# Performance work log

Hardware: AMD Instinct MI355X
Metric: run time of the kernel (lower is better)

The kernel has to match this reference:

```python
import jax, jax.numpy as jnp
import numpy as np

B, S, D, H = 8, 1024, 768, 16
PD = D // H  # projection dims per head


def setup_inputs() -> dict:
    key = jax.random.key(0)
    ks = jax.random.split(key, 9)
    s = 1.0 / np.sqrt(D)
    return {
        "inputs": jax.random.normal(ks[0], (B, S, D), dtype=jnp.float32),
        "Wq": jax.random.normal(ks[1], (D, D), dtype=jnp.float32) * s,
        "bq": jnp.zeros((D,), dtype=jnp.float32),
        "Wk": jax.random.normal(ks[2], (D, D), dtype=jnp.float32) * s,
        "bk": jnp.zeros((D,), dtype=jnp.float32),
        "Wv": jax.random.normal(ks[3], (D, D), dtype=jnp.float32) * s,
        "bv": jnp.zeros((D,), dtype=jnp.float32),
        "Wo": jax.random.normal(ks[4], (D, D), dtype=jnp.float32) * s,
        "bo": jnp.zeros((D,), dtype=jnp.float32),
    }


def _split_heads(x):
    # [B,S,D] -> [B,H,S,PD]
    return x.reshape(B, S, H, PD).transpose(0, 2, 1, 3)


def reference(inputs, Wq, bq, Wk, bk, Wv, bv, Wo, bo):
    q = _split_heads(inputs @ Wq + bq)
    k = _split_heads(inputs @ Wk + bk)
    v = _split_heads(inputs @ Wv + bv)
    scale = 1.0 / jnp.sqrt(jnp.asarray(PD, dtype=q.dtype))
    scores = jnp.einsum("bhqd,bhkd->bhqk", q, k) * scale
    weights = jax.nn.softmax(scores, axis=-1)
    attn = jnp.einsum("bhqk,bhkd->bhqd", weights, v)
    concat = attn.transpose(0, 2, 1, 3).reshape(B, S, D)
    return concat @ Wo + bo
```

## Files before the change

kernel.cpp:

```cpp
#include <hip/hip_runtime.h>
#include <hip/hip_bf16.h>

#define B_   8
#define S_   1024
#define D_   768
#define H_   16
#define PD_  48
#define PDP  64
#define M_   8192
#define BH_  128

#define QSCALE 0.20823031f

typedef __attribute__((ext_vector_type(8))) short short8;
typedef __attribute__((ext_vector_type(4))) float floatx4;

__device__ __forceinline__ unsigned short f2bf(float f) {
    return (unsigned short)((__float_as_uint(f) + 0x8000u) >> 16);
}
__device__ __forceinline__ unsigned int pack_bf2(float lo, float hi) {
    unsigned a = __float_as_uint(hi) + 0x8000u;
    unsigned b = __float_as_uint(lo) + 0x8000u;
    return __builtin_amdgcn_perm(a, b, 0x07060302u);
}

__device__ __forceinline__ void async_copy16(const unsigned short* gptr, unsigned short* lptr) {
    __builtin_amdgcn_global_load_lds(
        (const __attribute__((address_space(1))) unsigned int*)gptr,
        (__attribute__((address_space(3))) unsigned int*)lptr, 16, 0, 0);
}

__global__ __launch_bounds__(256) void prep_kernel(
    const float* __restrict__ X, unsigned short* __restrict__ Xb,
    const float* __restrict__ w0, const float* __restrict__ w1,
    const float* __restrict__ w2, const float* __restrict__ w3,
    unsigned short* __restrict__ Wtall) {
    __shared__ float tile[32][33];
    const int tid = threadIdx.x;
    const int bx = blockIdx.x;
    if (bx < 6144) {
        long i = ((long)bx * 256 + tid) * 4;
        float4 v = *(const float4*)(X + i);
        uint2 o;
        o.x = pack_bf2(v.x, v.y);
        o.y = pack_bf2(v.z, v.w);
        *(uint2*)(Xb + i) = o;
        return;
    }
    const int t = bx - 6144;
    const int z = t / 576, r = t % 576;
    const int nt = (r % 24) * 32, kt = (r / 24) * 32;
    const int tx = tid & 31, ty = tid >> 5;
    const float* W = (z == 0) ? w0 : (z == 1) ? w1 : (z == 2) ? w2 : w3;
    unsigned short* Wt = Wtall + (long)z * D_ * D_;
#pragma unroll
    for (int i = 0; i < 4; i++)
        tile[ty + i * 8][tx] = W[(long)(kt + ty + i * 8) * D_ + nt + tx];
    __syncthreads();
#pragma unroll
    for (int i = 0; i < 4; i++)
        Wt[(long)(nt + ty + i * 8) * D_ + kt + tx] = f2bf(tile[tx][ty + i * 8]);
}

__device__ __forceinline__ void gemm_core(
    const unsigned short* __restrict__ Ag,
    const unsigned short* __restrict__ Btg,
    unsigned short* Asm, unsigned short* Bsm, floatx4 acc[4][4]) {
    const int tid = threadIdx.x;
    const int lane = tid & 63, w = tid >> 6;
    const int wr = (w >> 1) * 64, wc = (w & 1) * 64;
    const int l15 = lane & 15, l4 = lane >> 4;
    const floatx4 zero = {0.f, 0.f, 0.f, 0.f};
#pragma unroll
    for (int mt = 0; mt < 4; mt++)
#pragma unroll
        for (int nt = 0; nt < 4; nt++) acc[mt][nt] = zero;

    for (int kb = 0; kb < D_; kb += 64) {
#pragma unroll
        for (int i = 0; i < 4; i++) {
            int c = tid + i * 256;
            int row = c >> 3, seg = (c & 7) ^ (row & 7);
            long goff = (long)row * D_ + kb + seg * 8;
            async_copy16(&Ag[goff], &Asm[c * 8]);
            async_copy16(&Btg[goff], &Bsm[c * 8]);
        }
        __syncthreads();
#pragma unroll
        for (int kk = 0; kk < 2; kk++) {
            short8 af[4], bf[4];
#pragma unroll
            for (int mt = 0; mt < 4; mt++) {
                int r = wr + mt * 16 + l15;
                af[mt] = *(const short8*)&Asm[r * 64 + (((kk * 4 + l4) ^ (r & 7)) * 8)];
            }
#pragma unroll
            for (int nt = 0; nt < 4; nt++) {
                int c = wc + nt * 16 + l15;
                bf[nt] = *(const short8*)&Bsm[c * 64 + (((kk * 4 + l4) ^ (c & 7)) * 8)];
            }
#pragma unroll
            for (int mt = 0; mt < 4; mt++)
#pragma unroll
                for (int nt = 0; nt < 4; nt++)
                    acc[mt][nt] = __builtin_amdgcn_mfma_f32_16x16x32_bf16(
                        af[mt], bf[nt], acc[mt][nt], 0, 0, 0);
        }
        __syncthreads();
    }
}

__global__ __launch_bounds__(256) void gemm_qkv_kernel(
    const unsigned short* __restrict__ Xb, const unsigned short* __restrict__ Wtall,
    const float* __restrict__ bq, const float* __restrict__ bk,
    const float* __restrict__ bv, unsigned short* __restrict__ QKV) {
    __shared__ __align__(16) unsigned short Asm[128 * 64];
    __shared__ __align__(16) unsigned short Bsm[128 * 64];
    const int z = blockIdx.z;
    const int m0 = blockIdx.x * 128, n0 = blockIdx.y * 128;
    const float* bias = (z == 0) ? bq : (z == 1) ? bk : bv;
    const float vscale = (z == 0) ? QSCALE : 1.0f;
    floatx4 acc[4][4];
    gemm_core(Xb + (long)m0 * D_, Wtall + (long)z * D_ * D_ + (long)n0 * D_, Asm, Bsm, acc);

    unsigned short* out = QKV + (long)z * BH_ * S_ * PDP;
    const int tid = threadIdx.x, lane = tid & 63, w = tid >> 6;
    const int wr = (w >> 1) * 64, wc = (w & 1) * 64;
    const int l15 = lane & 15, l4 = lane >> 4;
    const int b = m0 >> 10, sbase = m0 & 1023;
#pragma unroll
    for (int nt = 0; nt < 4; nt++) {
        int n = n0 + wc + nt * 16 + l15;
        int h = n / PD_, pd = n % PD_;
        float bb = bias[n];
#pragma unroll
        for (int mt = 0; mt < 4; mt++) {
#pragma unroll
            for (int r = 0; r < 4; r++) {
                int s = sbase + wr + mt * 16 + l4 * 4 + r;
                out[((long)(b * H_ + h) * S_ + s) * PDP + pd] = f2bf((acc[mt][nt][r] + bb) * vscale);
            }
        }
    }
}

__global__ __launch_bounds__(256) void transpose_v_kernel(
    const unsigned short* __restrict__ V, unsigned short* __restrict__ Vt) {
    __shared__ __align__(16) unsigned short T[64 * 64];
    const int tid = threadIdx.x;
    const int st = blockIdx.x * 64, bh = blockIdx.y;
    const unsigned short* src = V + (long)bh * S_ * PDP;
    unsigned short* dst = Vt + (long)bh * PDP * S_;
#pragma unroll
    for (int i = 0; i < 2; i++) {
        int c = tid + i * 256;
        int row = c >> 3, seg = (c & 7) ^ (row & 7);
        async_copy16(&src[(long)(st + row) * PDP + seg * 8], &T[c * 8]);
    }
    __syncthreads();
    const int d = tid >> 2;
    unsigned short tmp[16];
#pragma unroll
    for (int j = 0; j < 16; j++) {
        int sl = (tid & 3) * 16 + j;
        unsigned short v = T[sl * 64 + ((d >> 3) ^ (sl & 7)) * 8 + (d & 7)];
        tmp[j] = (d < PD_) ? v : ((d == PD_) ? (unsigned short)0x3F80 : (unsigned short)0);
    }
    *(uint4*)&dst[(long)d * S_ + st + (tid & 3) * 16] = *(uint4*)&tmp[0];
    *(uint4*)&dst[(long)d * S_ + st + (tid & 3) * 16 + 8] = *(uint4*)&tmp[8];
}

__global__ __launch_bounds__(256) void gemm_out_kernel(
    const unsigned short* __restrict__ Ctx, const unsigned short* __restrict__ Wot,
    const float* __restrict__ bo, float* __restrict__ Out) {
    __shared__ __align__(16) unsigned short Asm[128 * 64];
    __shared__ __align__(16) unsigned short Bsm[128 * 64];
    const int m0 = blockIdx.x * 128, n0 = blockIdx.y * 128;
    floatx4 acc[4][4];
    gemm_core(Ctx + (long)m0 * D_, Wot + (long)n0 * D_, Asm, Bsm, acc);

    const int tid = threadIdx.x, lane = tid & 63, w = tid >> 6;
    const int wr = (w >> 1) * 64, wc = (w & 1) * 64;
    const int l15 = lane & 15, l4 = lane >> 4;
#pragma unroll
    for (int nt = 0; nt < 4; nt++) {
        int n = n0 + wc + nt * 16 + l15;
        float bb = bo[n];
#pragma unroll
        for (int mt = 0; mt < 4; mt++) {
#pragma unroll
            for (int r = 0; r < 4; r++) {
                int m = m0 + wr + mt * 16 + l4 * 4 + r;
                Out[(long)m * D_ + n] = acc[mt][nt][r] + bb;
            }
        }
    }
}

__global__ __launch_bounds__(256) void attn_kernel(
    const unsigned short* __restrict__ Qg, const unsigned short* __restrict__ Kg,
    const unsigned short* __restrict__ Vtg, unsigned short* __restrict__ Ctx) {
    __shared__ __align__(16) unsigned short Ps[4][64 * 64];
    const int tid = threadIdx.x, lane = tid & 63, w = tid >> 6;
    const int l15 = lane & 15, l4 = lane >> 4;
    const int bh = blockIdx.x, qt = blockIdx.y;
    const long qkbase = (long)bh * S_ * PDP;
    const long vbase  = (long)bh * PDP * S_;

    short8 bq[4][2];
#pragma unroll
    for (int g = 0; g < 4; g++) {
        int qrow = qt * 256 + w * 64 + g * 16 + l15;
        bq[g][0] = *(const short8*)&Qg[qkbase + (long)qrow * PDP + l4 * 8];
        bq[g][1] = *(const short8*)&Qg[qkbase + (long)qrow * PDP + 32 + l4 * 8];
    }
    if (l4 >= 2) {
        const short8 z8 = {0, 0, 0, 0, 0, 0, 0, 0};
#pragma unroll
        for (int g = 0; g < 4; g++) bq[g][1] = z8;
    }

    const floatx4 zero = {0.f, 0.f, 0.f, 0.f};
    floatx4 accO[4][4];
#pragma unroll
    for (int g = 0; g < 4; g++)
#pragma unroll
        for (int nt = 0; nt < 4; nt++) accO[g][nt] = zero;

    unsigned short* Pw = &Ps[w][0];

    for (int kt = 0; kt < 16; kt++) {
        short8 ak[4][2];
#pragma unroll
        for (int ks = 0; ks < 4; ks++) {
            const unsigned short* kr = &Kg[qkbase + (long)(kt * 64 + ks * 16 + l15) * PDP];
            ak[ks][0] = *(const short8*)&kr[l4 * 8];
            ak[ks][1] = *(const short8*)&kr[32 + l4 * 8];
        }

#pragma unroll
        for (int g = 0; g < 4; g++) {
            floatx4 sc[4];
#pragma unroll
            for (int ks = 0; ks < 4; ks++) {
                floatx4 a = zero;
                a = __builtin_amdgcn_mfma_f32_16x16x32_bf16(ak[ks][0], bq[g][0], a, 0, 0, 0);
                a = __builtin_amdgcn_mfma_f32_16x16x32_bf16(ak[ks][1], bq[g][1], a, 0, 0, 0);
                sc[ks] = a;
            }
            int prow = g * 16 + l15;
#pragma unroll
            for (int ks = 0; ks < 4; ks++) {
                uint2 pp;
                pp.x = pack_bf2(__builtin_amdgcn_exp2f(sc[ks][0]),
                                __builtin_amdgcn_exp2f(sc[ks][1]));
                pp.y = pack_bf2(__builtin_amdgcn_exp2f(sc[ks][2]),
                                __builtin_amdgcn_exp2f(sc[ks][3]));
                int addr = prow * 64 + (((ks * 2 + (l4 >> 1)) ^ (prow & 7)) * 8) + (l4 & 1) * 4;
                *(uint2*)&Pw[addr] = pp;
            }
        }

#pragma unroll
        for (int kk = 0; kk < 2; kk++) {
            short8 bv[4];
#pragma unroll
            for (int nt = 0; nt < 4; nt++) {
                int d = nt * 16 + l15;
                bv[nt] = *(const short8*)&Vtg[vbase + (long)d * S_ + kt * 64 + kk * 32 + l4 * 8];
            }
#pragma unroll
            for (int g = 0; g < 4; g++) {
                int prow = g * 16 + l15;
                short8 ap = *(const short8*)&Pw[prow * 64 + (((kk * 4 + l4) ^ (prow & 7)) * 8)];
#pragma unroll
                for (int nt = 0; nt < 4; nt++)
                    accO[g][nt] = __builtin_amdgcn_mfma_f32_16x16x32_bf16(ap, bv[nt], accO[g][nt], 0, 0, 0);
            }
        }
    }

    const int b = bh >> 4, h = bh & 15;
#pragma unroll
    for (int g = 0; g < 4; g++) {
#pragma unroll
        for (int r = 0; r < 4; r++) {
            float lsum = __shfl(accO[g][3][r], lane & 48);
            float inv = 1.0f / lsum;
            int q = qt * 256 + w * 64 + g * 16 + l4 * 4 + r;
            long rowoff = (long)(b * S_ + q) * D_ + h * PD_;
#pragma unroll
            for (int nt = 0; nt < 3; nt++)
                Ctx[rowoff + nt * 16 + l15] = f2bf(accO[g][nt][r] * inv);
        }
    }
}

extern "C" void kernel_launch(void* const* d_in, const int* in_sizes, int n_in,
                              void* d_out, int out_size, void* d_ws, size_t ws_size,
                              hipStream_t stream) {
    const float* X  = (const float*)d_in[0];
    const float* Wq = (const float*)d_in[1];
    const float* bq = (const float*)d_in[2];
    const float* Wk = (const float*)d_in[3];
    const float* bk = (const float*)d_in[4];
    const float* Wv = (const float*)d_in[5];
    const float* bv = (const float*)d_in[6];
    const float* Wo = (const float*)d_in[7];
    const float* bo = (const float*)d_in[8];

    unsigned char* ws = (unsigned char*)d_ws;
    const long XB_BYTES  = (long)M_ * D_ * 2;
    const long WT_BYTES  = (long)D_ * D_ * 2;
    const long QKV_BYTES = (long)BH_ * S_ * PDP * 2;

    unsigned short* Xbf   = (unsigned short*)(ws);
    unsigned short* Wtall = (unsigned short*)(ws + XB_BYTES);
    unsigned short* Qws   = (unsigned short*)(ws + XB_BYTES + 4 * WT_BYTES);
    unsigned short* Kws   = Qws + QKV_BYTES / 2;
    unsigned short* Vws   = Kws + QKV_BYTES / 2;
    unsigned short* Vtws  = Vws + QKV_BYTES / 2;
    unsigned short* Ctx   = Vws;

    prep_kernel<<<8448, 256, 0, stream>>>(X, Xbf, Wq, Wk, Wv, Wo, Wtall);
    gemm_qkv_kernel<<<dim3(64, 6, 3), 256, 0, stream>>>(Xbf, Wtall, bq, bk, bv, Qws);
    transpose_v_kernel<<<dim3(16, 128), 256, 0, stream>>>(Vws, Vtws);
    attn_kernel<<<dim3(128, 4), 256, 0, stream>>>(Qws, Kws, Vtws, Ctx);
    gemm_out_kernel<<<dim3(64, 6), 256, 0, stream>>>(
        Ctx, Wtall + 3 * (WT_BYTES / 2), bo, (float*)d_out);
}
```

Before: 223.4 us.

## Stage K/V tiles in LDS with double buffering and vectorize epilogue stores

The attention kernel now loads K and V^T tiles cooperatively into double-buffered, XOR-swizzled shared memory using async copies, prefetching the next tile while the current one is computed. Previously each wave read K and V^T directly from global memory. MFMA operands are swapped in the GEMMs and in the PV product so each lane holds four consecutive columns of a row, which lets the QKV, output and context epilogues use vectorized 8- or 16-byte stores instead of scalar ones. This adds 32KB of LDS and a barrier per iteration, and sets launch_bounds to 2 blocks per CU, which may limit occupancy.

```diff
diff --git a/kernel.cpp b/kernel.cpp
--- a/kernel.cpp
+++ b/kernel.cpp
@@ -104,7 +104,7 @@
 #pragma unroll
                 for (int nt = 0; nt < 4; nt++)
                     acc[mt][nt] = __builtin_amdgcn_mfma_f32_16x16x32_bf16(
-                        af[mt], bf[nt], acc[mt][nt], 0, 0, 0);
+                        bf[nt], af[mt], acc[mt][nt], 0, 0, 0);
         }
         __syncthreads();
     }
@@ -130,16 +130,17 @@
     const int b = m0 >> 10, sbase = m0 & 1023;
 #pragma unroll
     for (int nt = 0; nt < 4; nt++) {
-        int n = n0 + wc + nt * 16 + l15;
-        int h = n / PD_, pd = n % PD_;
-        float bb = bias[n];
+        int nq = n0 + wc + nt * 16 + l4 * 4;
+        int h = nq / PD_, pd0 = nq % PD_;
+        float4 bb = *(const float4*)&bias[nq];
+        long hbase = (long)(b * H_ + h) * S_;
 #pragma unroll
         for (int mt = 0; mt < 4; mt++) {
-#pragma unroll
-            for (int r = 0; r < 4; r++) {
-                int s = sbase + wr + mt * 16 + l4 * 4 + r;
-                out[((long)(b * H_ + h) * S_ + s) * PDP + pd] = f2bf((acc[mt][nt][r] + bb) * vscale);
-            }
+            int s = sbase + wr + mt * 16 + l15;
+            uint2 pp;
+            pp.x = pack_bf2((acc[mt][nt][0] + bb.x) * vscale, (acc[mt][nt][1] + bb.y) * vscale);
+            pp.y = pack_bf2((acc[mt][nt][2] + bb.z) * vscale, (acc[mt][nt][3] + bb.w) * vscale);
+            *(uint2*)&out[(hbase + s) * PDP + pd0] = pp;
         }
     }
 }
@@ -184,22 +185,24 @@
     const int l15 = lane & 15, l4 = lane >> 4;
 #pragma unroll
     for (int nt = 0; nt < 4; nt++) {
-        int n = n0 + wc + nt * 16 + l15;
-        float bb = bo[n];
+        int nq = n0 + wc + nt * 16 + l4 * 4;
+        float4 bb = *(const float4*)&bo[nq];
 #pragma unroll
         for (int mt = 0; mt < 4; mt++) {
-#pragma unroll
-            for (int r = 0; r < 4; r++) {
-                int m = m0 + wr + mt * 16 + l4 * 4 + r;
-                Out[(long)m * D_ + n] = acc[mt][nt][r] + bb;
-            }
-        }
-    }
-}
-
-__global__ __launch_bounds__(256) void attn_kernel(
+            int m = m0 + wr + mt * 16 + l15;
+            float4 o;
+            o.x = acc[mt][nt][0] + bb.x; o.y = acc[mt][nt][1] + bb.y;
+            o.z = acc[mt][nt][2] + bb.z; o.w = acc[mt][nt][3] + bb.w;
+            *(float4*)&Out[(long)m * D_ + nq] = o;
+        }
+    }
+}
+
+__global__ __launch_bounds__(256, 2) void attn_kernel(
     const unsigned short* __restrict__ Qg, const unsigned short* __restrict__ Kg,
     const unsigned short* __restrict__ Vtg, unsigned short* __restrict__ Ctx) {
+    __shared__ __align__(16) unsigned short Ks[2][64 * 64];
+    __shared__ __align__(16) unsigned short Vs[2][64 * 64];
     __shared__ __align__(16) unsigned short Ps[4][64 * 64];
     const int tid = threadIdx.x, lane = tid & 63, w = tid >> 6;
     const int l15 = lane & 15, l4 = lane >> 4;
@@ -207,6 +210,15 @@
     const long qkbase = (long)bh * S_ * PDP;
     const long vbase  = (long)bh * PDP * S_;
 
+    const int c0 = tid, c1 = tid + 256;
+    const int row0 = c0 >> 3, seg0 = (c0 & 7) ^ (row0 & 7);
+    const int row1 = c1 >> 3, seg1 = (c1 & 7) ^ (row1 & 7);
+
+    async_copy16(&Kg[qkbase + (long)row0 * PDP + seg0 * 8], &Ks[0][c0 * 8]);
+    async_copy16(&Kg[qkbase + (long)row1 * PDP + seg1 * 8], &Ks[0][c1 * 8]);
+    async_copy16(&Vtg[vbase + (long)row0 * S_ + seg0 * 8], &Vs[0][c0 * 8]);
+    async_copy16(&Vtg[vbase + (long)row1 * S_ + seg1 * 8], &Vs[0][c1 * 8]);
+
     short8 bq[4][2];
 #pragma unroll
     for (int g = 0; g < 4; g++) {
@@ -230,12 +242,24 @@
     unsigned short* Pw = &Ps[w][0];
 
     for (int kt = 0; kt < 16; kt++) {
+        const int cur = kt & 1;
+        __syncthreads();
+        if (kt < 15) {
+            const int nb = cur ^ 1;
+            const long krow = qkbase + (long)(kt + 1) * 64 * PDP;
+            const int vcol = (kt + 1) * 64;
+            async_copy16(&Kg[krow + (long)row0 * PDP + seg0 * 8], &Ks[nb][c0 * 8]);
+            async_copy16(&Kg[krow + (long)row1 * PDP + seg1 * 8], &Ks[nb][c1 * 8]);
+            async_copy16(&Vtg[vbase + (long)row0 * S_ + vcol + seg0 * 8], &Vs[nb][c0 * 8]);
+            async_copy16(&Vtg[vbase + (long)row1 * S_ + vcol + seg1 * 8], &Vs[nb][c1 * 8]);
+        }
+
         short8 ak[4][2];
 #pragma unroll
         for (int ks = 0; ks < 4; ks++) {
-            const unsigned short* kr = &Kg[qkbase + (long)(kt * 64 + ks * 16 + l15) * PDP];
-            ak[ks][0] = *(const short8*)&kr[l4 * 8];
-            ak[ks][1] = *(const short8*)&kr[32 + l4 * 8];
+            int kr = ks * 16 + l15;
+            ak[ks][0] = *(const short8*)&Ks[cur][kr * 64 + ((l4 ^ (kr & 7)) * 8)];
+            ak[ks][1] = *(const short8*)&Ks[cur][kr * 64 + (((4 + l4) ^ (kr & 7)) * 8)];
         }
 
 #pragma unroll
@@ -263,19 +287,19 @@
 
 #pragma unroll
         for (int kk = 0; kk < 2; kk++) {
-            short8 bv[4];
+            short8 av[4];
 #pragma unroll
             for (int nt = 0; nt < 4; nt++) {
-                int d = nt * 16 + l15;
-                bv[nt] = *(const short8*)&Vtg[vbase + (long)d * S_ + kt * 64 + kk * 32 + l4 * 8];
+                int vr = nt * 16 + l15;
+                av[nt] = *(const short8*)&Vs[cur][vr * 64 + (((kk * 4 + l4) ^ (vr & 7)) * 8)];
             }
 #pragma unroll
             for (int g = 0; g < 4; g++) {
                 int prow = g * 16 + l15;
-                short8 ap = *(const short8*)&Pw[prow * 64 + (((kk * 4 + l4) ^ (prow & 7)) * 8)];
+                short8 bp = *(const short8*)&Pw[prow * 64 + (((kk * 4 + l4) ^ (prow & 7)) * 8)];
 #pragma unroll
                 for (int nt = 0; nt < 4; nt++)
-                    accO[g][nt] = __builtin_amdgcn_mfma_f32_16x16x32_bf16(ap, bv[nt], accO[g][nt], 0, 0, 0);
+                    accO[g][nt] = __builtin_amdgcn_mfma_f32_16x16x32_bf16(av[nt], bp, accO[g][nt], 0, 0, 0);
             }
         }
     }
@@ -283,15 +307,16 @@
     const int b = bh >> 4, h = bh & 15;
 #pragma unroll
     for (int g = 0; g < 4; g++) {
-#pragma unroll
-        for (int r = 0; r < 4; r++) {
-            float lsum = __shfl(accO[g][3][r], lane & 48);
-            float inv = 1.0f / lsum;
-            int q = qt * 256 + w * 64 + g * 16 + l4 * 4 + r;
-            long rowoff = (long)(b * S_ + q) * D_ + h * PD_;
-#pragma unroll
-            for (int nt = 0; nt < 3; nt++)
-                Ctx[rowoff + nt * 16 + l15] = f2bf(accO[g][nt][r] * inv);
+        float lsum = __shfl(accO[g][3][0], l15);
+        float inv = 1.0f / lsum;
+        int q = qt * 256 + w * 64 + g * 16 + l15;
+        long rowoff = (long)(b * S_ + q) * D_ + h * PD_ + l4 * 4;
+#pragma unroll
+        for (int nt = 0; nt < 3; nt++) {
+            uint2 pp;
+            pp.x = pack_bf2(accO[g][nt][0] * inv, accO[g][nt][1] * inv);
+            pp.y = pack_bf2(accO[g][nt][2] * inv, accO[g][nt][3] * inv);
+            *(uint2*)&Ctx[rowoff + nt * 16] = pp;
         }
     }
 }
```

Result: faster. 209.3 us (-6.3%).
